# Kernel tuning notes

Measured on AMD Instinct MI355X. Metric: run time of the kernel, lower is better.

## Reference

```python
import jax, jax.numpy as jnp
import numpy as np

H = 1024
V = 50257
N = 4096
IGNORE_INDEX = -100


def setup_inputs() -> dict:
    key = jax.random.key(0)
    k1, k2, k3 = jax.random.split(key, 3)
    x = jax.random.normal(k1, (N, H), dtype=jnp.float32)
    weight = jax.random.normal(k2, (V, H), dtype=jnp.float32) * (H ** -0.5)
    target = jax.random.randint(k3, (N,), 0, V, dtype=jnp.int32)
    return {"x": x, "target": target, "weight": weight}


def reference(x, target, weight):
    # Fused LM head + cross-entropy (math-equivalent unfused form).
    logits = jnp.einsum("nh,vh->nv", x, weight)  # [N, V]
    logz = jax.nn.logsumexp(logits, axis=-1)     # [N]
    safe_tgt = jnp.where(target == IGNORE_INDEX, 0, target)
    picked = jnp.take_along_axis(logits, safe_tgt[:, None].astype(jnp.int32), axis=-1)[:, 0]
    valid = target != IGNORE_INDEX
    per_tok = jnp.where(valid, logz - picked, 0.0)
    n_valid = jnp.maximum(jnp.sum(valid), 1)
    return jnp.sum(per_tok) / n_valid.astype(per_tok.dtype)
```

## Files before the change

kernel.cpp:

```cpp
#include <hip/hip_runtime.h>
#include <hip/hip_bf16.h>
#include <hip/hip_fp8.h>

#define N_TOK 4096
#define H_DIM 1024
#define V_DIM 50257
#define IGNORE_IDX (-100)

#define BM 128
#define BN 128
#define BK 128
#define NSTEP (H_DIM / BK)
#define NCHUNK ((V_DIM + BN - 1) / BN)

#define LDT 72

typedef __attribute__((ext_vector_type(8))) short bf16x8;
typedef __attribute__((ext_vector_type(4))) float f32x4;

union Pack8 { __hip_bfloat162 h2[4]; int4 v; };

__device__ __forceinline__ void gload16(const void* g, void* l) {
    __builtin_amdgcn_global_load_lds(
        (const __attribute__((address_space(1))) unsigned int*)g,
        (__attribute__((address_space(3))) unsigned int*)l,
        16, 0, 0);
}

__device__ __forceinline__ int pack4_fp8(float a, float b, float c, float d) {
#if __has_builtin(__builtin_amdgcn_cvt_pk_fp8_f32)
    int w = __builtin_amdgcn_cvt_pk_fp8_f32(a, b, 0, false);
    w = __builtin_amdgcn_cvt_pk_fp8_f32(c, d, w, true);
    return w;
#else
    __hip_fp8_e4m3 q0(a), q1(b), q2(c), q3(d);
    return (int)q0.__x | ((int)q1.__x << 8) | ((int)q2.__x << 16) | ((int)q3.__x << 24);
#endif
}

__global__ __launch_bounds__(256) void cvt_x8_kernel(const float* __restrict__ x,
                                                     unsigned char* __restrict__ xb8) {
    size_t e = (size_t)blockIdx.x * 256 + threadIdx.x;
    const float4* s = reinterpret_cast<const float4*>(x) + e * 4;
    float4 f0 = s[0], f1 = s[1], f2 = s[2], f3 = s[3];
    int4 o;
    o.x = pack4_fp8(f0.x, f0.y, f0.z, f0.w);
    o.y = pack4_fp8(f1.x, f1.y, f1.z, f1.w);
    o.z = pack4_fp8(f2.x, f2.y, f2.z, f2.w);
    o.w = pack4_fp8(f3.x, f3.y, f3.z, f3.w);
    reinterpret_cast<int4*>(xb8)[e] = o;
}

__global__ __launch_bounds__(256) void cvt_w8_kernel(const float* __restrict__ W,
                                                     unsigned char* __restrict__ Wb8) {
    const size_t total = (size_t)V_DIM * H_DIM / 16;
    size_t stride = (size_t)gridDim.x * 256;
    for (size_t e = (size_t)blockIdx.x * 256 + threadIdx.x; e < total; e += stride) {
        const float4* s = reinterpret_cast<const float4*>(W) + e * 4;
        float4 f0 = s[0], f1 = s[1], f2 = s[2], f3 = s[3];
        int4 o;
        o.x = pack4_fp8(f0.x, f0.y, f0.z, f0.w);
        o.y = pack4_fp8(f1.x, f1.y, f1.z, f1.w);
        o.z = pack4_fp8(f2.x, f2.y, f2.z, f2.w);
        o.w = pack4_fp8(f3.x, f3.y, f3.z, f3.w);
        reinterpret_cast<int4*>(Wb8)[e] = o;
    }
}

__global__ __launch_bounds__(256, 4) void ce_gemm_fp8(
        const unsigned char* __restrict__ xb8,
        const unsigned char* __restrict__ Wb8,
        const int* __restrict__ tgt,
        float2* __restrict__ partials,
        float* __restrict__ picked) {
    __shared__ __align__(16) char lA[BM * BK];
    __shared__ __align__(16) char lB[BN * BK];
    __shared__ float2 mergebuf[BM][2];
    __shared__ int ltgt[BM];

    const int tid  = threadIdx.x;
    const int mb   = blockIdx.x;
    const int vb   = blockIdx.y;
    const int rbase = mb * BM;
    const int cbase = vb * BN;
    const int lane = tid & 63;
    const int wid  = tid >> 6;
    const int wr   = wid >> 1;
    const int wc   = wid & 1;
    const int l15  = lane & 15;
    const int lg   = lane >> 4;

    if (tid < BM) ltgt[tid] = tgt[rbase + tid];

    const unsigned char* srcA[4];
    const unsigned char* srcB[4];
    #pragma unroll
    for (int it = 0; it < 4; ++it) {
        int G = it * 256 + tid;
        int r = G >> 3, g = G & 7;
        int gs = g ^ (r & 7);
        srcA[it] = xb8 + (size_t)(rbase + r) * H_DIM + gs * 16;
        int vr = cbase + r; if (vr >= V_DIM) vr = V_DIM - 1;
        srcB[it] = Wb8 + (size_t)vr * H_DIM + gs * 16;
    }

    f32x4 acc[4][4] = {};

    for (int s = 0; s < NSTEP; ++s) {
        const int k0 = s * BK;
        __syncthreads();
        #pragma unroll
        for (int it = 0; it < 4; ++it) {
            gload16(srcA[it] + k0, lA + (it * 256 + wid * 64) * 16);
            gload16(srcB[it] + k0, lB + (it * 256 + wid * 64) * 16);
        }
        __syncthreads();
        #pragma unroll
        for (int kk = 0; kk < 4; ++kk) {
            long a[4], b[4];
            #pragma unroll
            for (int m = 0; m < 4; ++m) {
                int r = wr * 64 + m * 16 + l15;
                int slot = (kk * 2 + (lg >> 1)) ^ (r & 7);
                a[m] = *reinterpret_cast<const long*>(lA + r * 128 + (slot << 4) + (lg & 1) * 8);
            }
            #pragma unroll
            for (int n = 0; n < 4; ++n) {
                int r = wc * 64 + n * 16 + l15;
                int slot = (kk * 2 + (lg >> 1)) ^ (r & 7);
                b[n] = *reinterpret_cast<const long*>(lB + r * 128 + (slot << 4) + (lg & 1) * 8);
            }
            #pragma unroll
            for (int m = 0; m < 4; ++m)
                #pragma unroll
                for (int n = 0; n < 4; ++n)
                    acc[m][n] = __builtin_amdgcn_mfma_f32_16x16x32_fp8_fp8(a[m], b[n], acc[m][n], 0, 0, 0);
        }
    }

    #pragma unroll
    for (int m = 0; m < 4; ++m) {
        #pragma unroll
        for (int j = 0; j < 4; ++j) {
            int rl = wr * 64 + m * 16 + lg * 4 + j;
            int tg = ltgt[rl];
            float v4[4];
            float vmax = -INFINITY;
            #pragma unroll
            for (int n = 0; n < 4; ++n) {
                int cg = cbase + wc * 64 + n * 16 + l15;
                float val = acc[m][n][j];
                bool ok = cg < V_DIM;
                v4[n] = ok ? val : -INFINITY;
                if (ok && tg == cg) picked[rbase + rl] = val;
                vmax = fmaxf(vmax, v4[n]);
            }
            #pragma unroll
            for (int msk = 1; msk <= 8; msk <<= 1)
                vmax = fmaxf(vmax, __shfl_xor(vmax, msk));
            float ssum = 0.f;
            #pragma unroll
            for (int n = 0; n < 4; ++n)
                ssum += (v4[n] == -INFINITY) ? 0.f : __expf(v4[n] - vmax);
            #pragma unroll
            for (int msk = 1; msk <= 8; msk <<= 1)
                ssum += __shfl_xor(ssum, msk);
            if (l15 == 0) mergebuf[rl][wc] = make_float2(vmax, ssum);
        }
    }
    __syncthreads();
    if (tid < BM) {
        float2 p0 = mergebuf[tid][0], p1 = mergebuf[tid][1];
        float M = fmaxf(p0.x, p1.x);
        float sm = 0.f;
        if (p0.x > -INFINITY) sm += p0.y * __expf(p0.x - M);
        if (p1.x > -INFINITY) sm += p1.y * __expf(p1.x - M);
        partials[(size_t)(rbase + tid) * NCHUNK + vb] = make_float2(M, sm);
    }
}

__global__ __launch_bounds__(256) void cvt_x_kernel(const float* __restrict__ x,
                                                    __hip_bfloat16* __restrict__ xb) {
    size_t e = (size_t)blockIdx.x * 256 + threadIdx.x;
    const float4* s = reinterpret_cast<const float4*>(x) + e * 2;
    float4 a = s[0], b = s[1];
    Pack8 p;
    p.h2[0] = __float22bfloat162_rn(make_float2(a.x, a.y));
    p.h2[1] = __float22bfloat162_rn(make_float2(a.z, a.w));
    p.h2[2] = __float22bfloat162_rn(make_float2(b.x, b.y));
    p.h2[3] = __float22bfloat162_rn(make_float2(b.z, b.w));
    reinterpret_cast<int4*>(xb)[e] = p.v;
}

__global__ __launch_bounds__(256) void ce_gemm_kernel(
        const __hip_bfloat16* __restrict__ xb, const float* __restrict__ W,
        const int* __restrict__ tgt, float2* __restrict__ partials, float* __restrict__ picked) {
    __shared__ __hip_bfloat16 lA[BM * LDT];
    __shared__ __hip_bfloat16 lB[BN * LDT];
    __shared__ float2 mergebuf[BM][2];
    __shared__ int ltgt[BM];
    const int tid = threadIdx.x, mb = blockIdx.x, vb = blockIdx.y;
    const int rbase = mb * BM, cbase = vb * BN;
    const int lane = tid & 63, wid = tid >> 6;
    const int wr = wid >> 1, wc = wid & 1, l15 = lane & 15, lg = lane >> 4;
    if (tid < BM) ltgt[tid] = tgt[rbase + tid];
    f32x4 acc[4][4] = {};
    for (int s = 0; s < H_DIM / 64; ++s) {
        const int k0 = s * 64;
        __syncthreads();
        #pragma unroll
        for (int it = 0; it < 4; ++it) {
            int e = it * 256 + tid, r = e >> 3, c8 = e & 7;
            int4 v = *reinterpret_cast<const int4*>(xb + (size_t)(rbase + r) * H_DIM + k0 + c8 * 8);
            *reinterpret_cast<int4*>(&lA[r * LDT + c8 * 8]) = v;
        }
        #pragma unroll
        for (int it = 0; it < 4; ++it) {
            int e = it * 256 + tid, r = e >> 3, c8 = e & 7;
            int v = cbase + r; if (v >= V_DIM) v = V_DIM - 1;
            const float4* src = reinterpret_cast<const float4*>(W + (size_t)v * H_DIM + k0 + c8 * 8);
            float4 f0 = src[0], f1 = src[1];
            Pack8 p;
            p.h2[0] = __float22bfloat162_rn(make_float2(f0.x, f0.y));
            p.h2[1] = __float22bfloat162_rn(make_float2(f0.z, f0.w));
            p.h2[2] = __float22bfloat162_rn(make_float2(f1.x, f1.y));
            p.h2[3] = __float22bfloat162_rn(make_float2(f1.z, f1.w));
            *reinterpret_cast<int4*>(&lB[r * LDT + c8 * 8]) = p.v;
        }
        __syncthreads();
        #pragma unroll
        for (int kk = 0; kk < 2; ++kk) {
            bf16x8 af[4], bfr[4];
            #pragma unroll
            for (int m = 0; m < 4; ++m)
                af[m] = *reinterpret_cast<const bf16x8*>(&lA[(wr * 64 + m * 16 + l15) * LDT + kk * 32 + lg * 8]);
            #pragma unroll
            for (int n = 0; n < 4; ++n)
                bfr[n] = *reinterpret_cast<const bf16x8*>(&lB[(wc * 64 + n * 16 + l15) * LDT + kk * 32 + lg * 8]);
            #pragma unroll
            for (int m = 0; m < 4; ++m)
                #pragma unroll
                for (int n = 0; n < 4; ++n)
                    acc[m][n] = __builtin_amdgcn_mfma_f32_16x16x32_bf16(af[m], bfr[n], acc[m][n], 0, 0, 0);
        }
    }
    #pragma unroll
    for (int m = 0; m < 4; ++m) {
        #pragma unroll
        for (int j = 0; j < 4; ++j) {
            int rl = wr * 64 + m * 16 + lg * 4 + j;
            int tg = ltgt[rl];
            float v4[4]; float vmax = -INFINITY;
            #pragma unroll
            for (int n = 0; n < 4; ++n) {
                int cg = cbase + wc * 64 + n * 16 + l15;
                float val = acc[m][n][j];
                bool ok = cg < V_DIM;
                v4[n] = ok ? val : -INFINITY;
                if (ok && tg == cg) picked[rbase + rl] = val;
                vmax = fmaxf(vmax, v4[n]);
            }
            #pragma unroll
            for (int msk = 1; msk <= 8; msk <<= 1) vmax = fmaxf(vmax, __shfl_xor(vmax, msk));
            float ssum = 0.f;
            #pragma unroll
            for (int n = 0; n < 4; ++n) ssum += (v4[n] == -INFINITY) ? 0.f : __expf(v4[n] - vmax);
            #pragma unroll
            for (int msk = 1; msk <= 8; msk <<= 1) ssum += __shfl_xor(ssum, msk);
            if (l15 == 0) mergebuf[rl][wc] = make_float2(vmax, ssum);
        }
    }
    __syncthreads();
    if (tid < BM) {
        float2 p0 = mergebuf[tid][0], p1 = mergebuf[tid][1];
        float M = fmaxf(p0.x, p1.x);
        float sm = 0.f;
        if (p0.x > -INFINITY) sm += p0.y * __expf(p0.x - M);
        if (p1.x > -INFINITY) sm += p1.y * __expf(p1.x - M);
        partials[(size_t)(rbase + tid) * NCHUNK + vb] = make_float2(M, sm);
    }
}

__global__ __launch_bounds__(256) void ce_combine_kernel(
        const float2* __restrict__ partials, const float* __restrict__ picked,
        const int* __restrict__ tgt, float2* __restrict__ blockSums, int nchunk) {
    __shared__ float2 wsum[4];
    int tid = threadIdx.x, lane = tid & 63, wave = tid >> 6;
    int w = blockIdx.x * 4 + wave;
    float sum = 0.f, cnt = 0.f;
    for (int row = w; row < N_TOK; row += 256) {
        float m = -INFINITY, sacc = 0.f;
        for (int c = lane; c < nchunk; c += 64) {
            float2 p = partials[(size_t)row * nchunk + c];
            float M = fmaxf(m, p.x);
            sacc = sacc * __expf(m - M) + p.y * __expf(p.x - M);
            m = M;
        }
        #pragma unroll
        for (int msk = 1; msk < 64; msk <<= 1) {
            float om = __shfl_xor(m, msk), os = __shfl_xor(sacc, msk);
            float M = fmaxf(m, om);
            sacc = sacc * __expf(m - M) + os * __expf(om - M);
            m = M;
        }
        if (lane == 0) {
            int t = tgt[row];
            if (t != IGNORE_IDX) { sum += (m + __logf(sacc)) - picked[row]; cnt += 1.f; }
        }
    }
    if (lane == 0) wsum[wave] = make_float2(sum, cnt);
    __syncthreads();
    if (tid == 0) {
        float S = 0.f, C = 0.f;
        #pragma unroll
        for (int i = 0; i < 4; ++i) { S += wsum[i].x; C += wsum[i].y; }
        blockSums[blockIdx.x] = make_float2(S, C);
    }
}

__global__ void ce_final_kernel(const float2* __restrict__ blockSums, float* __restrict__ out) {
    int lane = threadIdx.x;
    float2 p = blockSums[lane];
    float S = p.x, C = p.y;
    #pragma unroll
    for (int msk = 1; msk < 64; msk <<= 1) { S += __shfl_xor(S, msk); C += __shfl_xor(C, msk); }
    if (lane == 0) out[0] = S / fmaxf(C, 1.f);
}

extern "C" void kernel_launch(void* const* d_in, const int* in_sizes, int n_in,
                              void* d_out, int out_size, void* d_ws, size_t ws_size,
                              hipStream_t stream) {
    const float* x   = (const float*)d_in[0];
    const int*   tgt = (const int*)d_in[1];
    const float* W   = (const float*)d_in[2];
    float* out = (float*)d_out;
    char* ws = (char*)d_ws;

    if (ws_size >= ((size_t)80 << 20)) {
        unsigned char* xb8 = (unsigned char*)ws;
        unsigned char* Wb8 = (unsigned char*)(ws + ((size_t)8 << 20));
        float2* partials   = (float2*)(ws + ((size_t)60 << 20));
        float*  picked     = (float*)(ws + ((size_t)76 << 20));
        float2* blockSums  = (float2*)(ws + ((size_t)77 << 20));

        cvt_x8_kernel<<<(N_TOK * H_DIM) / (256 * 16), 256, 0, stream>>>(x, xb8);
        cvt_w8_kernel<<<2048, 256, 0, stream>>>(W, Wb8);
        dim3 grid(N_TOK / BM, NCHUNK);
        ce_gemm_fp8<<<grid, 256, 0, stream>>>(xb8, Wb8, tgt, partials, picked);
        ce_combine_kernel<<<64, 256, 0, stream>>>(partials, picked, tgt, blockSums, NCHUNK);
        ce_final_kernel<<<1, 64, 0, stream>>>(blockSums, out);
    } else {
        __hip_bfloat16* xb = (__hip_bfloat16*)ws;
        float2* partials   = (float2*)(ws + (8u << 20));
        float*  picked     = (float*)(ws + (21u << 20));
        float2* blockSums  = (float2*)(ws + (21u << 20) + (64u << 10));

        cvt_x_kernel<<<(N_TOK * H_DIM) / (256 * 8), 256, 0, stream>>>(x, xb);
        dim3 grid(N_TOK / BM, NCHUNK);
        ce_gemm_kernel<<<grid, 256, 0, stream>>>(xb, W, tgt, partials, picked);
        ce_combine_kernel<<<64, 256, 0, stream>>>(partials, picked, tgt, blockSums, NCHUNK);
        ce_final_kernel<<<1, 64, 0, stream>>>(blockSums, out);
    }
}
```

Measured before the change: 444.1 us.

## Permute K-order in fp8 conversion so GEMM loads 16-byte LDS vectors

The fp8 conversion kernels now write x and W with the K dimension permuted inside each 128-element block, so each lane's MFMA operands for all four k-substeps sit in two contiguous 16-byte chunks. The GEMM inner loop then issues 2 wide LDS reads per fragment per step instead of 4 8-byte reads, with LDS offsets hoisted out of the K loop. This cuts LDS instruction count and address arithmetic, at the cost of more live registers and a less contiguous read pattern in the conversion kernels. The permutation is applied identically to both operands, so the dot product is unchanged.

```diff
diff --git a/kernel.cpp b/kernel.cpp
--- a/kernel.cpp
+++ b/kernel.cpp
@@ -17,6 +17,7 @@
 
 typedef __attribute__((ext_vector_type(8))) short bf16x8;
 typedef __attribute__((ext_vector_type(4))) float f32x4;
+typedef long longx2 __attribute__((ext_vector_type(2)));
 
 union Pack8 { __hip_bfloat162 h2[4]; int4 v; };
 
@@ -38,32 +39,42 @@
 #endif
 }
 
-__global__ __launch_bounds__(256) void cvt_x8_kernel(const float* __restrict__ x,
-                                                     unsigned char* __restrict__ xb8) {
-    size_t e = (size_t)blockIdx.x * 256 + threadIdx.x;
-    const float4* s = reinterpret_cast<const float4*>(x) + e * 4;
-    float4 f0 = s[0], f1 = s[1], f2 = s[2], f3 = s[3];
-    int4 o;
-    o.x = pack4_fp8(f0.x, f0.y, f0.z, f0.w);
-    o.y = pack4_fp8(f1.x, f1.y, f1.z, f1.w);
-    o.z = pack4_fp8(f2.x, f2.y, f2.z, f2.w);
-    o.w = pack4_fp8(f3.x, f3.y, f3.z, f3.w);
-    reinterpret_cast<int4*>(xb8)[e] = o;
-}
-
-__global__ __launch_bounds__(256) void cvt_w8_kernel(const float* __restrict__ W,
-                                                     unsigned char* __restrict__ Wb8) {
+__global__ __launch_bounds__(256) void cvt_x8p_kernel(const float* __restrict__ x,
+                                                      unsigned char* __restrict__ xb8) {
+    size_t E = (size_t)blockIdx.x * 256 + threadIdx.x;
+    int o = (int)(E & 7);
+    size_t blk = E >> 3;
+    const float* s = x + (blk << 7) + ((size_t)(o >> 2) << 6) + ((o & 3) << 3);
+    float4 f0 = *(const float4*)(s);
+    float4 f1 = *(const float4*)(s + 4);
+    float4 f2 = *(const float4*)(s + 32);
+    float4 f3 = *(const float4*)(s + 36);
+    int4 out;
+    out.x = pack4_fp8(f0.x, f0.y, f0.z, f0.w);
+    out.y = pack4_fp8(f1.x, f1.y, f1.z, f1.w);
+    out.z = pack4_fp8(f2.x, f2.y, f2.z, f2.w);
+    out.w = pack4_fp8(f3.x, f3.y, f3.z, f3.w);
+    reinterpret_cast<int4*>(xb8)[E] = out;
+}
+
+__global__ __launch_bounds__(256) void cvt_w8p_kernel(const float* __restrict__ W,
+                                                      unsigned char* __restrict__ Wb8) {
     const size_t total = (size_t)V_DIM * H_DIM / 16;
     size_t stride = (size_t)gridDim.x * 256;
-    for (size_t e = (size_t)blockIdx.x * 256 + threadIdx.x; e < total; e += stride) {
-        const float4* s = reinterpret_cast<const float4*>(W) + e * 4;
-        float4 f0 = s[0], f1 = s[1], f2 = s[2], f3 = s[3];
-        int4 o;
-        o.x = pack4_fp8(f0.x, f0.y, f0.z, f0.w);
-        o.y = pack4_fp8(f1.x, f1.y, f1.z, f1.w);
-        o.z = pack4_fp8(f2.x, f2.y, f2.z, f2.w);
-        o.w = pack4_fp8(f3.x, f3.y, f3.z, f3.w);
-        reinterpret_cast<int4*>(Wb8)[e] = o;
+    for (size_t E = (size_t)blockIdx.x * 256 + threadIdx.x; E < total; E += stride) {
+        int o = (int)(E & 7);
+        size_t blk = E >> 3;
+        const float* s = W + (blk << 7) + ((size_t)(o >> 2) << 6) + ((o & 3) << 3);
+        float4 f0 = *(const float4*)(s);
+        float4 f1 = *(const float4*)(s + 4);
+        float4 f2 = *(const float4*)(s + 32);
+        float4 f3 = *(const float4*)(s + 36);
+        int4 out;
+        out.x = pack4_fp8(f0.x, f0.y, f0.z, f0.w);
+        out.y = pack4_fp8(f1.x, f1.y, f1.z, f1.w);
+        out.z = pack4_fp8(f2.x, f2.y, f2.z, f2.w);
+        out.w = pack4_fp8(f3.x, f3.y, f3.z, f3.w);
+        reinterpret_cast<int4*>(Wb8)[E] = out;
     }
 }
 
@@ -104,6 +115,18 @@
         srcB[it] = Wb8 + (size_t)vr * H_DIM + gs * 16;
     }
 
+    int aoffb[4], boffb[4];
+    #pragma unroll
+    for (int m = 0; m < 4; ++m) {
+        int r = wr * 64 + m * 16 + l15;
+        aoffb[m] = r * 128 + ((lg ^ (r & 7)) << 4);
+    }
+    #pragma unroll
+    for (int n = 0; n < 4; ++n) {
+        int r = wc * 64 + n * 16 + l15;
+        boffb[n] = r * 128 + ((lg ^ (r & 7)) << 4);
+    }
+
     f32x4 acc[4][4] = {};
 
     for (int s = 0; s < NSTEP; ++s) {
@@ -115,27 +138,26 @@
             gload16(srcB[it] + k0, lB + (it * 256 + wid * 64) * 16);
         }
         __syncthreads();
-        #pragma unroll
-        for (int kk = 0; kk < 4; ++kk) {
-            long a[4], b[4];
-            #pragma unroll
-            for (int m = 0; m < 4; ++m) {
-                int r = wr * 64 + m * 16 + l15;
-                int slot = (kk * 2 + (lg >> 1)) ^ (r & 7);
-                a[m] = *reinterpret_cast<const long*>(lA + r * 128 + (slot << 4) + (lg & 1) * 8);
-            }
-            #pragma unroll
-            for (int n = 0; n < 4; ++n) {
-                int r = wc * 64 + n * 16 + l15;
-                int slot = (kk * 2 + (lg >> 1)) ^ (r & 7);
-                b[n] = *reinterpret_cast<const long*>(lB + r * 128 + (slot << 4) + (lg & 1) * 8);
-            }
+
+        longx2 va[4][2], vb[4][2];
+        #pragma unroll
+        for (int m = 0; m < 4; ++m) {
+            va[m][0] = *reinterpret_cast<const longx2*>(lA + aoffb[m]);
+            va[m][1] = *reinterpret_cast<const longx2*>(lA + (aoffb[m] ^ 64));
+        }
+        #pragma unroll
+        for (int n = 0; n < 4; ++n) {
+            vb[n][0] = *reinterpret_cast<const longx2*>(lB + boffb[n]);
+            vb[n][1] = *reinterpret_cast<const longx2*>(lB + (boffb[n] ^ 64));
+        }
+        #pragma unroll
+        for (int kk = 0; kk < 4; ++kk)
             #pragma unroll
             for (int m = 0; m < 4; ++m)
                 #pragma unroll
                 for (int n = 0; n < 4; ++n)
-                    acc[m][n] = __builtin_amdgcn_mfma_f32_16x16x32_fp8_fp8(a[m], b[n], acc[m][n], 0, 0, 0);
-        }
+                    acc[m][n] = __builtin_amdgcn_mfma_f32_16x16x32_fp8_fp8(
+                        va[m][kk >> 1][kk & 1], vb[n][kk >> 1][kk & 1], acc[m][n], 0, 0, 0);
     }
 
     #pragma unroll
@@ -343,8 +365,8 @@
         float*  picked     = (float*)(ws + ((size_t)76 << 20));
         float2* blockSums  = (float2*)(ws + ((size_t)77 << 20));
 
-        cvt_x8_kernel<<<(N_TOK * H_DIM) / (256 * 16), 256, 0, stream>>>(x, xb8);
-        cvt_w8_kernel<<<2048, 256, 0, stream>>>(W, Wb8);
+        cvt_x8p_kernel<<<(N_TOK * H_DIM) / (256 * 16), 256, 0, stream>>>(x, xb8);
+        cvt_w8p_kernel<<<2048, 256, 0, stream>>>(W, Wb8);
         dim3 grid(N_TOK / BM, NCHUNK);
         ce_gemm_fp8<<<grid, 256, 0, stream>>>(xb8, Wb8, tgt, partials, picked);
         ce_combine_kernel<<<64, 256, 0, stream>>>(partials, picked, tgt, blockSums, NCHUNK);
```

After: 399.3 us (median of 3 runs). 10.1% less time.
